# Kernel tuning notes

Measured on AMD Instinct MI355X. Metric: run time of the kernel, lower is better.

Reference implementation:

```python
import jax, jax.numpy as jnp
import numpy as np

IMG, P, CIN, D, K, L, H, FF, B = 512, 32, 3, 256, 8192, 6, 8, 1024, 32
GRID = IMG // P  # 16
DH = D // H
EPS = 1e-5


def _ln(x, w, b):
    m = x.mean(-1, keepdims=True)
    v = ((x - m) ** 2).mean(-1, keepdims=True)
    return (x - m) / jnp.sqrt(v + EPS) * w + b


def _mha(x, wqkv, bqkv, wo, bo):
    # x: (S, Bt, D) -- axis 0 is the attention axis (torch batch_first=False quirk)
    S, Bt, _ = x.shape
    qkv = x @ wqkv.T + bqkv
    q, k, v = jnp.split(qkv, 3, axis=-1)
    q = q.reshape(S, Bt, H, DH)
    k = k.reshape(S, Bt, H, DH)
    v = v.reshape(S, Bt, H, DH)
    scores = jnp.einsum('sbhd,tbhd->bhst', q, k) / jnp.sqrt(jnp.float32(DH))
    attn = jax.nn.softmax(scores, axis=-1)
    o = jnp.einsum('bhst,tbhd->sbhd', attn, v).reshape(S, Bt, D)
    return o @ wo.T + bo


def _conv_t(x, w, b, stride=2, pad=1):
    # w uses torch ConvTranspose2d layout (Cin, Cout, kH, kW)
    kH = w.shape[2]
    wf = jnp.flip(w, (2, 3)).transpose(1, 0, 2, 3)  # -> (Cout, Cin, kH, kW)
    y = jax.lax.conv_general_dilated(
        x, wf, window_strides=(1, 1),
        padding=[(kH - 1 - pad, kH - 1 - pad)] * 2,
        lhs_dilation=(stride, stride),
        dimension_numbers=('NCHW', 'OIHW', 'NCHW'))
    return y + b[None, :, None, None]


def _forward(x, patch_w, patch_b, qkv_w, qkv_b, out_w, out_b, ln1_w, ln1_b,
             ln2_w, ln2_b, ff1_w, ff1_b, ff2_w, ff2_b, lnf_w, lnf_b, codebook,
             dec_w0, dec_b0, dec_w1, dec_b1, dec_w2, dec_b2, dec_w3, dec_b3):
    # patch embedding: conv stride=patch -> (B, D, G, G) -> (B, N, D)
    h = jax.lax.conv_general_dilated(
        x, patch_w, (P, P), 'VALID',
        dimension_numbers=('NCHW', 'OIHW', 'NCHW')) + patch_b[None, :, None, None]
    h = h.reshape(h.shape[0], D, -1).transpose(0, 2, 1)  # (B, N, D)
    # torch TransformerEncoderLayer default batch_first=False: attention runs
    # over axis 0 (image batch); faithfully replicated here. Post-norm, eval
    # mode (dropout=identity), exact gelu.
    for i in range(L):
        a = _mha(h, qkv_w[i], qkv_b[i], out_w[i], out_b[i])
        h = _ln(h + a, ln1_w[i], ln1_b[i])
        f = jax.nn.gelu(h @ ff1_w[i].T + ff1_b[i], approximate=False) @ ff2_w[i].T + ff2_b[i]
        h = _ln(h + f, ln2_w[i], ln2_b[i])
    h = _ln(h, lnf_w, lnf_b)
    # vector quantization: squared-distance argmin over codebook
    flat = h.reshape(-1, D)  # (B*N, D)
    d = ((flat ** 2).sum(-1, keepdims=True)
         - 2.0 * flat @ codebook.T
         + (codebook ** 2).sum(-1))  # (B*N, K)
    idx = jnp.argmin(d, axis=1)
    q = codebook[idx].reshape(h.shape)
    e_loss = jnp.mean((jax.lax.stop_gradient(q) - h) ** 2)
    q_loss = jnp.mean((q - jax.lax.stop_gradient(h)) ** 2)
    vq_loss = q_loss + 0.25 * e_loss
    q = h + jax.lax.stop_gradient(q - h)  # straight-through
    q = q.transpose(0, 2, 1).reshape(x.shape[0], D, GRID, GRID)
    y = jax.nn.relu(_conv_t(q, dec_w0, dec_b0))
    y = jax.nn.relu(_conv_t(y, dec_w1, dec_b1))
    y = jax.nn.relu(_conv_t(y, dec_w2, dec_b2))
    x_hat = jax.nn.sigmoid(_conv_t(y, dec_w3, dec_b3))
    return x_hat, vq_loss


def setup_inputs() -> dict:
    key = jax.random.key(0)
    ks = iter(jax.random.split(key, 64))
    nrm = lambda shape, s=0.02: jax.random.normal(next(ks), shape, jnp.float32) * s
    f32 = jnp.float32
    return {
        'x': jax.random.normal(next(ks), (B, CIN, IMG, IMG), f32),
        'patch_w': nrm((D, CIN, P, P)),
        'patch_b': jnp.zeros((D,), f32),
        'qkv_w': nrm((L, 3 * D, D)),
        'qkv_b': jnp.zeros((L, 3 * D), f32),
        'out_w': nrm((L, D, D)),
        'out_b': jnp.zeros((L, D), f32),
        'ln1_w': jnp.ones((L, D), f32),
        'ln1_b': jnp.zeros((L, D), f32),
        'ln2_w': jnp.ones((L, D), f32),
        'ln2_b': jnp.zeros((L, D), f32),
        'ff1_w': nrm((L, FF, D)),
        'ff1_b': jnp.zeros((L, FF), f32),
        'ff2_w': nrm((L, D, FF)),
        'ff2_b': jnp.zeros((L, D), f32),
        'lnf_w': jnp.ones((D,), f32),
        'lnf_b': jnp.zeros((D,), f32),
        'codebook': jax.random.uniform(next(ks), (K, D), f32, -1.0 / K, 1.0 / K),
        'dec_w0': nrm((D, 256, 4, 4)),
        'dec_b0': jnp.zeros((256,), f32),
        'dec_w1': nrm((256, 128, 4, 4)),
        'dec_b1': jnp.zeros((128,), f32),
        'dec_w2': nrm((128, 64, 4, 4)),
        'dec_b2': jnp.zeros((64,), f32),
        'dec_w3': nrm((64, CIN, 4, 4)),
        'dec_b3': jnp.zeros((CIN,), f32),
    }


def reference(x, patch_w, patch_b, qkv_w, qkv_b, out_w, out_b, ln1_w, ln1_b,
              ln2_w, ln2_b, ff1_w, ff1_b, ff2_w, ff2_b, lnf_w, lnf_b, codebook,
              dec_w0, dec_b0, dec_w1, dec_b1, dec_w2, dec_b2, dec_w3, dec_b3):
    return _forward(x, patch_w, patch_b, qkv_w, qkv_b, out_w, out_b, ln1_w,
                    ln1_b, ln2_w, ln2_b, ff1_w, ff1_b, ff2_w, ff2_b, lnf_w,
                    lnf_b, codebook, dec_w0, dec_b0, dec_w1, dec_b1, dec_w2,
                    dec_b2, dec_w3, dec_b3)
```

## Files before the change

kernel.cpp:

```cpp
#include <hip/hip_runtime.h>
#include <hip/hip_bf16.h>
#include <math.h>

typedef __hip_bfloat16 bf16;
typedef unsigned int u32;
typedef unsigned long long u64;
using short8 = __attribute__((ext_vector_type(8))) short;
using f32x4  = __attribute__((ext_vector_type(4))) float;

__device__ __forceinline__ float b2f(bf16 v){ return __bfloat162float(v); }
__device__ __forceinline__ bf16  f2b(float v){ return __float2bfloat16(v); }
__device__ __forceinline__ float plo(u32 u){ return __uint_as_float(u << 16); }
__device__ __forceinline__ float phi(u32 u){ return __uint_as_float(u & 0xffff0000u); }

__device__ __forceinline__ void gld16(const void* g, void* l)
{
  __builtin_amdgcn_global_load_lds(
      (const __attribute__((address_space(1))) u32*)g,
      (__attribute__((address_space(3))) u32*)l, 16, 0, 0);
}

__global__ void k_detect(const u32* probe, int* flag)
{
  if (threadIdx.x == 0 && blockIdx.x == 0)
    *flag = (*probe == 0x3F800000u) ? 0 : 1;
}

struct PPack { const void* s[25]; u32 off[26]; };
__global__ __launch_bounds__(256) void k_convall(PPack pp, bf16* P, const int* flag)
{
  const u32 i = blockIdx.x * 256 + threadIdx.x;
  if (i >= pp.off[25]) return;
  int lo = 0, hi = 25;
  while (hi - lo > 1) { const int mid = (lo + hi) >> 1; if (i >= pp.off[mid]) lo = mid; else hi = mid; }
  const u32 j = i - pp.off[lo];
  P[i] = *flag ? ((const bf16*)pp.s[lo])[j] : f2b(((const float*)pp.s[lo])[j]);
}

__global__ __launch_bounds__(256) void k_zborder(bf16* buf, int Hp, int C, int nimg)
{
  const int per = 4 * Hp - 4;
  const int c8 = C >> 3;
  const int total = nimg * per * c8;
  const int i = blockIdx.x * 256 + threadIdx.x;
  if (i >= total) return;
  const int ch8 = i % c8;
  const int pb = i / c8;
  const int img = pb / per;
  const int b = pb - img * per;
  int y, x;
  if (b < Hp) { y = 0; x = b; }
  else if (b < 2 * Hp) { y = Hp - 1; x = b - Hp; }
  else {
    const int r = b - 2 * Hp;
    const int side = r / (Hp - 2);
    y = 1 + r - side * (Hp - 2);
    x = side ? (Hp - 1) : 0;
  }
  uint4 z = {0, 0, 0, 0};
  *reinterpret_cast<uint4*>(buf + (((size_t)img * Hp + y) * Hp + x) * C + ch8 * 8) = z;
}

__global__ __launch_bounds__(128) void k_im2col(const void* x, bf16* A, const int* flag)
{
  const int m = blockIdx.y;
  const int k8 = blockIdx.x * 128 + threadIdx.x;
  const int k = k8 * 8;
  const int b = m >> 8, n = m & 255;
  const int gy = n >> 4, gx = n & 15;
  const int c = k >> 10, r = (k >> 5) & 31, pp = k & 31;
  const size_t src = (((size_t)(b * 3 + c) * 512) + gy * 32 + r) * 512 + gx * 32 + pp;
  bf16 ov[8];
  if (*flag) {
    const bf16* xp = (const bf16*)x + src;
    #pragma unroll
    for (int i = 0; i < 8; ++i) ov[i] = xp[i];
  } else {
    const float4 v0 = *reinterpret_cast<const float4*>((const float*)x + src);
    const float4 v1 = *reinterpret_cast<const float4*>((const float*)x + src + 4);
    ov[0]=f2b(v0.x); ov[1]=f2b(v0.y); ov[2]=f2b(v0.z); ov[3]=f2b(v0.w);
    ov[4]=f2b(v1.x); ov[5]=f2b(v1.y); ov[6]=f2b(v1.z); ov[7]=f2b(v1.w);
  }
  *reinterpret_cast<uint4*>(A + (size_t)m * 3072 + k) = *reinterpret_cast<const uint4*>(ov);
}

template<int EPI, int FM, int BN, bool DB>
__global__ __launch_bounds__(256, 2) void gemm_t(
    const bf16* __restrict__ A, const bf16* __restrict__ Bw,
    const bf16* __restrict__ bias, const bf16* res, bf16* C,
    const float* __restrict__ cnorm, u64* __restrict__ ku,
    int M, int N, int K, int Kc)
{
  constexpr int BM = FM * 32;
  constexpr int FN = BN / 32;
  __shared__ alignas(16) bf16 As[DB ? 2 : 1][BM * 64];
  __shared__ alignas(16) bf16 Bs[DB ? 2 : 1][BN * 64];
  const int tid = threadIdx.x;
  const int bn = blockIdx.x * BN, bm = blockIdx.y * BM;
  const int z = blockIdx.z;
  const int kb = z * Kc;
  const int l = tid & 63, w = tid >> 6;
  const int wm = w >> 1, wn = w & 1;
  const int lg = l >> 4, lr = l & 15;
  const int sr8 = l >> 3;
  const int sch = (l & 7) ^ sr8;
  f32x4 acc[FM][FN];
  #pragma unroll
  for (int fm = 0; fm < FM; ++fm)
    #pragma unroll
    for (int fn = 0; fn < FN; ++fn) acc[fm][fn] = (f32x4){0.f, 0.f, 0.f, 0.f};

  auto stage = [&](int bb, int k0) {
    char* ab = (char*)As[bb];
    char* bp = (char*)Bs[bb];
    #pragma unroll
    for (int it = 0; it < FM; ++it) {
      const int r = w * 8 + it * 32 + sr8;
      gld16(A + (size_t)(bm + r) * K + k0 + sch * 8, ab + w * 1024 + it * 4096);
    }
    #pragma unroll
    for (int it = 0; it < BN / 32; ++it) {
      const int r = w * 8 + it * 32 + sr8;
      gld16(Bw + (size_t)(bn + r) * K + k0 + sch * 8, bp + w * 1024 + it * 4096);
    }
  };
  auto compute = [&](int bb) {
    const char* ab = (const char*)As[bb];
    const char* bp = (const char*)Bs[bb];
    #pragma unroll
    for (int ks = 0; ks < 2; ++ks) {
      short8 af[FM], bfr[FN];
      #pragma unroll
      for (int fm = 0; fm < FM; ++fm) {
        const int r = wm * (FM * 16) + fm * 16 + lr;
        af[fm] = *reinterpret_cast<const short8*>(ab + r * 128 + (((lg + ks * 4) ^ (r & 7)) * 16));
      }
      #pragma unroll
      for (int fn = 0; fn < FN; ++fn) {
        const int r = wn * (BN / 2) + fn * 16 + lr;
        bfr[fn] = *reinterpret_cast<const short8*>(bp + r * 128 + (((lg + ks * 4) ^ (r & 7)) * 16));
      }
      #pragma unroll
      for (int fm = 0; fm < FM; ++fm)
        #pragma unroll
        for (int fn = 0; fn < FN; ++fn)
          acc[fm][fn] = __builtin_amdgcn_mfma_f32_16x16x32_bf16(af[fm], bfr[fn], acc[fm][fn], 0, 0, 0);
    }
  };

  const int nt = Kc >> 6;
  if (DB) {
    stage(0, kb);
    __syncthreads();
    for (int t = 0; t < nt; ++t) {
      const int cur = t & 1;
      if (t + 1 < nt) stage(cur ^ 1, kb + ((t + 1) << 6));
      compute(cur);
      __syncthreads();
    }
  } else {
    for (int t = 0; t < nt; ++t) {
      if (t) __syncthreads();
      stage(0, kb + (t << 6));
      __syncthreads();
      compute(0);
    }
  }

  if (EPI == 3) {
    __shared__ u64 skey[BM][2];
    float cn[FN];
    #pragma unroll
    for (int fn = 0; fn < FN; ++fn) cn[fn] = cnorm[bn + wn * (BN / 2) + fn * 16 + lr];
    #pragma unroll
    for (int fm = 0; fm < FM; ++fm) {
      #pragma unroll
      for (int r = 0; r < 4; ++r) {
        u64 best = ~0ull;
        #pragma unroll
        for (int fn = 0; fn < FN; ++fn) {
          const int col = bn + wn * (BN / 2) + fn * 16 + lr;
          const float d = cn[fn] - 2.0f * acc[fm][fn][r];
          u32 u = __float_as_uint(d);
          u = (u & 0x80000000u) ? ~u : (u | 0x80000000u);
          const u64 key = ((u64)u << 32) | (u32)col;
          best = key < best ? key : best;
        }
        #pragma unroll
        for (int mk = 1; mk < 16; mk <<= 1) {
          const u64 o = __shfl_xor(best, mk, 64);
          best = o < best ? o : best;
        }
        if (lr == 0) skey[wm * (FM * 16) + fm * 16 + lg * 4 + r][wn] = best;
      }
    }
    __syncthreads();
    if (tid < BM) {
      const u64 a = skey[tid][0], b = skey[tid][1];
      ku[(size_t)blockIdx.x * M + bm + tid] = a < b ? a : b;
    }
  } else if (EPI == 4) {
    #pragma unroll
    for (int fm = 0; fm < FM; ++fm) {
      const int m0 = bm + wm * (FM * 16) + fm * 16 + lg * 4;
      #pragma unroll
      for (int fn = 0; fn < FN; ++fn) {
        const int n = bn + wn * (BN / 2) + fn * 16 + lr;
        #pragma unroll
        for (int r = 0; r < 4; ++r)
          C[((size_t)z * M + m0 + r) * N + n] = f2b(acc[fm][fn][r]);
      }
    }
  } else {
    #pragma unroll
    for (int fm = 0; fm < FM; ++fm) {
      const int m0 = bm + wm * (FM * 16) + fm * 16 + lg * 4;
      #pragma unroll
      for (int fn = 0; fn < FN; ++fn) {
        const int n = bn + wn * (BN / 2) + fn * 16 + lr;
        const float bs = b2f(bias[n]);
        #pragma unroll
        for (int r = 0; r < 4; ++r) {
          float v = acc[fm][fn][r] + bs;
          if (EPI == 1) v = 0.5f * v * (1.0f + erff(v * 0.70710678118654752f));
          if (EPI == 2) v += b2f(res[(size_t)(m0 + r) * N + n]);
          C[(size_t)(m0 + r) * N + n] = f2b(v);
        }
      }
    }
  }
}

__global__ __launch_bounds__(256, 1) void k_fat1(
    bf16* __restrict__ hbuf,
    const bf16* __restrict__ Wqkv, const bf16* __restrict__ Bqkv,
    const bf16* __restrict__ Wo, const bf16* __restrict__ Bo,
    const bf16* __restrict__ lw, const bf16* __restrict__ lb)
{
  __shared__ alignas(16) bf16 hs[32 * 256];
  __shared__ alignas(16) bf16 ao[32 * 256];
  __shared__ alignas(16) bf16 astage[128 * 64];
  __shared__ bf16 att[3 * 9216];
  __shared__ float ps[32][33];
  __shared__ float rs[32];
  __shared__ float psum[32][4], psq[32][4];
  __shared__ float mstat[32], istat[32];

  const int bt = blockIdx.x;
  const int tid = threadIdx.x;
  const int l = tid & 63, w = tid >> 6;
  const int lg = l >> 4, lr = l & 15;
  const int sr8 = l >> 3;
  const int sch = (l & 7) ^ sr8;
  char* hsb = (char*)hs;
  char* aob = (char*)ao;
  char* asb = (char*)astage;

  #pragma unroll
  for (int call = 0; call < 4; ++call) {
    const int id = call * 256 + tid;
    const int s = id >> 5, within = id & 31;
    const int grp = within >> 3, c = within & 7;
    gld16(hbuf + (size_t)(s * 256 + bt) * 256 + grp * 64 + ((c ^ (s & 7)) * 8),
          hsb + call * 4096 + w * 1024);
  }

  for (int at = 0; at < 6; ++at) {
    f32x4 acc[2][2];
    #pragma unroll
    for (int fm = 0; fm < 2; ++fm)
      #pragma unroll
      for (int fn = 0; fn < 2; ++fn) acc[fm][fn] = (f32x4){0.f, 0.f, 0.f, 0.f};
    for (int kst = 0; kst < 4; ++kst) {
      __syncthreads();
      #pragma unroll
      for (int it = 0; it < 4; ++it) {
        const int r = w * 8 + it * 32 + sr8;
        gld16(Wqkv + (size_t)(at * 128 + r) * 256 + kst * 64 + sch * 8,
              asb + w * 1024 + it * 4096);
      }
      __syncthreads();
      #pragma unroll
      for (int ks = 0; ks < 2; ++ks) {
        short8 af[2], bfr[2];
        #pragma unroll
        for (int fm = 0; fm < 2; ++fm) {
          const int r = w * 32 + fm * 16 + lr;
          af[fm] = *reinterpret_cast<const short8*>(asb + r * 128 + (((lg + ks * 4) ^ (r & 7)) * 16));
        }
        #pragma unroll
        for (int fn = 0; fn < 2; ++fn) {
          const int sr = fn * 16 + lr;
          bfr[fn] = *reinterpret_cast<const short8*>(hsb + sr * 512 + kst * 128 + (((lg + ks * 4) ^ (sr & 7)) * 16));
        }
        #pragma unroll
        for (int fm = 0; fm < 2; ++fm)
          #pragma unroll
          for (int fn = 0; fn < 2; ++fn)
            acc[fm][fn] = __builtin_amdgcn_mfma_f32_16x16x32_bf16(af[fm], bfr[fn], acc[fm][fn], 0, 0, 0);
      }
    }
    #pragma unroll
    for (int fm = 0; fm < 2; ++fm) {
      #pragma unroll
      for (int fn = 0; fn < 2; ++fn) {
        const int s = fn * 16 + lr;
        #pragma unroll
        for (int r = 0; r < 4; ++r) {
          const int n = at * 128 + w * 32 + fm * 16 + lg * 4 + r;
          const int p = n >> 8, rem = n & 255;
          att[p * 9216 + (rem >> 5) * 1152 + s * 36 + (rem & 31)] =
              f2b(acc[fm][fn][r] + b2f(Bqkv[n]));
        }
      }
    }
  }
  __syncthreads();

  const int s_a = tid >> 3, j_a = tid & 7;
  for (int hd = 0; hd < 8; ++hd) {
    const bf16* qrow = att + hd * 1152 + s_a * 36;
    float sc[4];
    #pragma unroll
    for (int e = 0; e < 4; ++e) {
      const int t = j_a + 8 * e;
      const bf16* krow = att + 9216 + hd * 1152 + t * 36;
      float v = 0.f;
      #pragma unroll
      for (int dd = 0; dd < 32; ++dd) v += b2f(qrow[dd]) * b2f(krow[dd]);
      sc[e] = v * 0.17677669529663687f;
    }
    float mx = fmaxf(fmaxf(sc[0], sc[1]), fmaxf(sc[2], sc[3]));
    #pragma unroll
    for (int mk = 1; mk < 8; mk <<= 1) mx = fmaxf(mx, __shfl_xor(mx, mk, 64));
    float sm = 0.f; float ex[4];
    #pragma unroll
    for (int e = 0; e < 4; ++e) { ex[e] = expf(sc[e] - mx); sm += ex[e]; }
    #pragma unroll
    for (int mk = 1; mk < 8; mk <<= 1) sm += __shfl_xor(sm, mk, 64);
    #pragma unroll
    for (int e = 0; e < 4; ++e) ps[s_a][j_a + 8 * e] = ex[e];
    if (j_a == 0) rs[s_a] = 1.0f / sm;
    __syncthreads();
    const float rinv = rs[s_a];
    float av[4];
    #pragma unroll
    for (int e = 0; e < 4; ++e) {
      const int dd = j_a * 4 + e;
      float a = 0.f;
      #pragma unroll
      for (int t = 0; t < 32; ++t)
        a += ps[s_a][t] * b2f(att[2 * 9216 + hd * 1152 + t * 36 + dd]);
      av[e] = a * rinv;
    }
    alignas(8) bf16 ov[4];
    #pragma unroll
    for (int e = 0; e < 4; ++e) ov[e] = f2b(av[e]);
    const int clog = (hd & 1) * 4 + (j_a >> 1);
    *reinterpret_cast<ushort4*>(aob + s_a * 512 + (hd >> 1) * 128 +
        ((clog ^ (s_a & 7)) * 16) + (j_a & 1) * 8) =
        *reinterpret_cast<const ushort4*>(ov);
    __syncthreads();
  }

  float vals[2][2][2][4];
  for (int at = 0; at < 2; ++at) {
    f32x4 acc[2][2];
    #pragma unroll
    for (int fm = 0; fm < 2; ++fm)
      #pragma unroll
      for (int fn = 0; fn < 2; ++fn) acc[fm][fn] = (f32x4){0.f, 0.f, 0.f, 0.f};
    for (int kst = 0; kst < 4; ++kst) {
      __syncthreads();
      #pragma unroll
      for (int it = 0; it < 4; ++it) {
        const int r = w * 8 + it * 32 + sr8;
        gld16(Wo + (size_t)(at * 128 + r) * 256 + kst * 64 + sch * 8,
              asb + w * 1024 + it * 4096);
      }
      __syncthreads();
      #pragma unroll
      for (int ks = 0; ks < 2; ++ks) {
        short8 af[2], bfr[2];
        #pragma unroll
        for (int fm = 0; fm < 2; ++fm) {
          const int r = w * 32 + fm * 16 + lr;
          af[fm] = *reinterpret_cast<const short8*>(asb + r * 128 + (((lg + ks * 4) ^ (r & 7)) * 16));
        }
        #pragma unroll
        for (int fn = 0; fn < 2; ++fn) {
          const int sr = fn * 16 + lr;
          bfr[fn] = *reinterpret_cast<const short8*>(aob + sr * 512 + kst * 128 + (((lg + ks * 4) ^ (sr & 7)) * 16));
        }
        #pragma unroll
        for (int fm = 0; fm < 2; ++fm)
          #pragma unroll
          for (int fn = 0; fn < 2; ++fn)
            acc[fm][fn] = __builtin_amdgcn_mfma_f32_16x16x32_bf16(af[fm], bfr[fn], acc[fm][fn], 0, 0, 0);
      }
    }
    #pragma unroll
    for (int fm = 0; fm < 2; ++fm)
      #pragma unroll
      for (int fn = 0; fn < 2; ++fn)
        #pragma unroll
        for (int r = 0; r < 4; ++r) vals[at][fm][fn][r] = acc[fm][fn][r];
  }

  float s1[2] = {0.f, 0.f}, s2[2] = {0.f, 0.f};
  #pragma unroll
  for (int at = 0; at < 2; ++at) {
    #pragma unroll
    for (int fm = 0; fm < 2; ++fm) {
      const int n4 = at * 128 + w * 32 + fm * 16 + lg * 4;
      #pragma unroll
      for (int fn = 0; fn < 2; ++fn) {
        const int s = fn * 16 + lr;
        const ushort4 hr = *reinterpret_cast<const ushort4*>(
            hsb + s * 512 + (n4 >> 6) * 128 + ((((n4 >> 3) & 7) ^ (s & 7)) * 16) + (n4 & 7) * 2);
        const bf16* hb = reinterpret_cast<const bf16*>(&hr);
        #pragma unroll
        for (int r = 0; r < 4; ++r) {
          const float v = vals[at][fm][fn][r] + b2f(Bo[n4 + r]) + b2f(hb[r]);
          vals[at][fm][fn][r] = v;
          s1[fn] += v;
          s2[fn] += v * v;
        }
      }
    }
  }
  #pragma unroll
  for (int fn = 0; fn < 2; ++fn) {
    float a = s1[fn], b = s2[fn];
    a += __shfl_xor(a, 16, 64); a += __shfl_xor(a, 32, 64);
    b += __shfl_xor(b, 16, 64); b += __shfl_xor(b, 32, 64);
    if (lg == 0) { psum[fn * 16 + lr][w] = a; psq[fn * 16 + lr][w] = b; }
  }
  __syncthreads();
  if (tid < 32) {
    float sa = 0.f, sb = 0.f;
    #pragma unroll
    for (int k = 0; k < 4; ++k) { sa += psum[tid][k]; sb += psq[tid][k]; }
    const float m = sa * (1.0f / 256.0f);
    mstat[tid] = m;
    istat[tid] = 1.0f / sqrtf(sb * (1.0f / 256.0f) - m * m + 1e-5f);
  }
  __syncthreads();
  #pragma unroll
  for (int at = 0; at < 2; ++at) {
    #pragma unroll
    for (int fm = 0; fm < 2; ++fm) {
      const int n4 = at * 128 + w * 32 + fm * 16 + lg * 4;
      #pragma unroll
      for (int fn = 0; fn < 2; ++fn) {
        const int s = fn * 16 + lr;
        const float m = mstat[s], inv = istat[s];
        alignas(8) bf16 ov[4];
        #pragma unroll
        for (int r = 0; r < 4; ++r)
          ov[r] = f2b((vals[at][fm][fn][r] - m) * inv * b2f(lw[n4 + r]) + b2f(lb[n4 + r]));
        *reinterpret_cast<ushort4*>(hbuf + (size_t)(s * 256 + bt) * 256 + n4) =
            *reinterpret_cast<const ushort4*>(ov);
      }
    }
  }
}

template<bool DOLN>
__global__ __launch_bounds__(256) void k_lnred(
    const bf16* __restrict__ Pf, const bf16* __restrict__ bias,
    const bf16* res, const bf16* __restrict__ lw, const bf16* __restrict__ lb,
    bf16* h, int kc)
{
  __shared__ float red[256];
  __shared__ float stat[2];
  const int row = blockIdx.x, d = threadIdx.x;
  float s = 0.f;
  for (int z = 0; z < kc; ++z) s += b2f(Pf[((size_t)z * 8192 + row) * 256 + d]);
  s += b2f(bias[d]);
  if (res) s += b2f(res[(size_t)row * 256 + d]);
  if (!DOLN) { h[(size_t)row * 256 + d] = f2b(s); return; }
  red[d] = s;
  __syncthreads();
  for (int off = 128; off > 0; off >>= 1) {
    if (d < off) red[d] += red[d + off];
    __syncthreads();
  }
  if (d == 0) stat[0] = red[0] * (1.0f / 256.0f);
  __syncthreads();
  const float m = stat[0];
  red[d] = (s - m) * (s - m);
  __syncthreads();
  for (int off = 128; off > 0; off >>= 1) {
    if (d < off) red[d] += red[d + off];
    __syncthreads();
  }
  if (d == 0) stat[1] = 1.0f / sqrtf(red[0] * (1.0f / 256.0f) + 1e-5f);
  __syncthreads();
  h[(size_t)row * 256 + d] = f2b((s - m) * stat[1] * b2f(lw[d]) + b2f(lb[d]));
}

__global__ __launch_bounds__(256) void k_vqmerge(
    const u64* __restrict__ ku, int* __restrict__ idx, int M, int NB)
{
  const int r = blockIdx.x * 256 + threadIdx.x;
  if (r >= M) return;
  u64 best = ku[r];
  for (int nb = 1; nb < NB; ++nb) {
    const u64 k = ku[(size_t)nb * M + r];
    best = k < best ? k : best;
  }
  idx[r] = (int)(best & 0xFFFFFFFFull);
}

__global__ __launch_bounds__(256) void k_cnorm(const bf16* __restrict__ cb, float* __restrict__ cn)
{
  const int j = blockIdx.x * 256 + threadIdx.x;
  const u32* p = (const u32*)(cb + (size_t)j * 256);
  float s = 0.f;
  for (int k = 0; k < 128; ++k) {
    const u32 v = p[k];
    const float a = plo(v), b = phi(v);
    s += a * a + b * b;
  }
  cn[j] = s;
}

__global__ __launch_bounds__(256) void k_ln(
    bf16* h, const bf16* w, const bf16* b)
{
  __shared__ float red[256];
  __shared__ float stat[2];
  const int row = blockIdx.x, d = threadIdx.x;
  const size_t base = (size_t)row * 256;
  const float x = b2f(h[base + d]);
  red[d] = x;
  __syncthreads();
  for (int off = 128; off > 0; off >>= 1) {
    if (d < off) red[d] += red[d + off];
    __syncthreads();
  }
  if (d == 0) stat[0] = red[0] * (1.0f / 256.0f);
  __syncthreads();
  const float m = stat[0];
  red[d] = (x - m) * (x - m);
  __syncthreads();
  for (int off = 128; off > 0; off >>= 1) {
    if (d < off) red[d] += red[d + off];
    __syncthreads();
  }
  if (d == 0) stat[1] = 1.0f / sqrtf(red[0] * (1.0f / 256.0f) + 1e-5f);
  __syncthreads();
  h[base + d] = f2b((x - m) * stat[1] * b2f(w[d]) + b2f(b[d]));
}

__global__ __launch_bounds__(256) void k_gather(
    const bf16* h, const bf16* cb, const int* idx, bf16* a0, float* lsum)
{
  __shared__ float red[256];
  const int row = blockIdx.x, d = threadIdx.x;
  const int code = idx[row] & 8191;
  const float q = b2f(cb[(size_t)code * 256 + d]);
  const float x = b2f(h[(size_t)row * 256 + d]);
  red[d] = (q - x) * (q - x);
  __syncthreads();
  for (int off = 128; off > 0; off >>= 1) {
    if (d < off) red[d] += red[d + off];
    __syncthreads();
  }
  if (d == 0) lsum[row] = red[0];
  const int b = row >> 8, n = row & 255;
  const int y = n >> 4, xc = n & 15;
  a0[(((size_t)b * 18 + y + 1) * 18 + (xc + 1)) * 256 + d] = f2b(q);
}

__global__ __launch_bounds__(256) void k_loss(const float* lsum, float* out)
{
  __shared__ float red[256];
  const int tid = threadIdx.x;
  float v = 0.f;
  for (int i = 0; i < 32; ++i) v += lsum[tid + 256 * i];
  red[tid] = v;
  __syncthreads();
  for (int off = 128; off > 0; off >>= 1) {
    if (tid < off) red[tid] += red[tid + off];
    __syncthreads();
  }
  if (tid == 0)
    out[0] = red[0] * (1.25f / 2097152.0f);
}

__global__ __launch_bounds__(256) void k_wtrans(
    const bf16* __restrict__ w, bf16* __restrict__ wt,
    int Cin, int lCin, int CoutR, int CoutP)
{
  const int K = Cin << 2;
  const int total = 4 * CoutP * K;
  const int i = blockIdx.x * 256 + threadIdx.x;
  if (i >= total) return;
  const int p = i / (CoutP * K);
  const int rem = i - p * (CoutP * K);
  const int co = rem / K;
  const int k = rem - co * K;
  const int tap = k >> lCin, ci = k - (tap << lCin);
  const int py = p >> 1, px = p & 1, ty = tap >> 1, tx = tap & 1;
  bf16 v = f2b(0.f);
  if (co < CoutR)
    v = w[(((size_t)ci * CoutR + co) * 4 + py + 2 * ty) * 4 + px + 2 * tx];
  wt[i] = v;
}

__global__ __launch_bounds__(256, 2) void convt64(
    const bf16* __restrict__ in, const bf16* __restrict__ Wt,
    const bf16* __restrict__ bias, bf16* __restrict__ outp,
    int H, int lH, int Cin, int lCin, int Cout)
{
  __shared__ alignas(16) bf16 As[2][128 * 64];
  __shared__ alignas(16) bf16 Bs[2][64 * 64];
  const int tid = threadIdx.x;
  const int pz = blockIdx.z;
  const int py = pz >> 1, px = pz & 1;
  const int K = Cin << 2;
  const int bn = blockIdx.x * 64, bm = blockIdx.y * 128;
  const bf16* Bw = Wt + (size_t)pz * Cout * K;
  const int l = tid & 63, w = tid >> 6;
  const int wm = w >> 1, wn = w & 1;
  const int lg = l >> 4, lr = l & 15;
  const int sr8 = l >> 3;
  const int sch = (l & 7) ^ sr8;
  const int Hp = H + 2;
  f32x4 acc[4][2];
  #pragma unroll
  for (int fm = 0; fm < 4; ++fm)
    #pragma unroll
    for (int fn = 0; fn < 2; ++fn) acc[fm][fn] = (f32x4){0.f, 0.f, 0.f, 0.f};

  size_t pixbase[4];
  #pragma unroll
  for (int it = 0; it < 4; ++it) {
    const int m = bm + w * 8 + it * 32 + sr8;
    const int b = m >> (2 * lH);
    const int rem = m & ((1 << (2 * lH)) - 1);
    const int jj = rem >> lH, ii = rem & (H - 1);
    pixbase[it] = ((size_t)(b * Hp + jj) * Hp + ii);
  }

  auto stage = [&](int bb, int k0) {
    char* ab = (char*)As[bb];
    char* bp = (char*)Bs[bb];
    const int tap = k0 >> lCin;
    const int ty = tap >> 1, tx = tap & 1;
    const int sy = (1 - py) + (1 - ty);
    const int sx = (1 - px) + (1 - tx);
    const int ci0 = (k0 - (tap << lCin)) + sch * 8;
    #pragma unroll
    for (int it = 0; it < 4; ++it)
      gld16(in + (pixbase[it] + (size_t)sy * Hp + sx) * Cin + ci0,
            ab + w * 1024 + it * 4096);
    #pragma unroll
    for (int it = 0; it < 2; ++it) {
      const int r = w * 8 + it * 32 + sr8;
      gld16(Bw + (size_t)(bn + r) * K + k0 + sch * 8, bp + w * 1024 + it * 4096);
    }
  };

  const int nt = K >> 6;
  stage(0, 0);
  __syncthreads();
  for (int t = 0; t < nt; ++t) {
    const int cur = t & 1;
    if (t + 1 < nt) stage(cur ^ 1, (t + 1) << 6);
    const char* ab = (const char*)As[cur];
    const char* bb = (const char*)Bs[cur];
    #pragma unroll
    for (int ks = 0; ks < 2; ++ks) {
      short8 af[4], bfr[2];
      #pragma unroll
      for (int fm = 0; fm < 4; ++fm) {
        const int r = wm * 64 + fm * 16 + lr;
        af[fm] = *reinterpret_cast<const short8*>(ab + r * 128 + (((lg + ks * 4) ^ (r & 7)) * 16));
      }
      #pragma unroll
      for (int fn = 0; fn < 2; ++fn) {
        const int r = wn * 32 + fn * 16 + lr;
        bfr[fn] = *reinterpret_cast<const short8*>(bb + r * 128 + (((lg + ks * 4) ^ (r & 7)) * 16));
      }
      #pragma unroll
      for (int fm = 0; fm < 4; ++fm)
        #pragma unroll
        for (int fn = 0; fn < 2; ++fn)
          acc[fm][fn] = __builtin_amdgcn_mfma_f32_16x16x32_bf16(af[fm], bfr[fn], acc[fm][fn], 0, 0, 0);
    }
    __syncthreads();
  }

  const int Ho = 2 * H, Hop = Ho + 2;
  #pragma unroll
  for (int fm = 0; fm < 4; ++fm) {
    const int m0 = bm + wm * 64 + fm * 16 + lg * 4;
    #pragma unroll
    for (int fn = 0; fn < 2; ++fn) {
      const int n = bn + wn * 32 + fn * 16 + lr;
      #pragma unroll
      for (int r = 0; r < 4; ++r) {
        const int m = m0 + r;
        const int b = m >> (2 * lH);
        const int rem = m & ((1 << (2 * lH)) - 1);
        const int jj = rem >> lH, ii = rem & (H - 1);
        const int oy = 2 * jj + (1 - py), ox = 2 * ii + (1 - px);
        const float v = fmaxf(acc[fm][fn][r] + b2f(bias[n]), 0.f);
        outp[((size_t)(b * Hop + oy + 1) * Hop + ox + 1) * Cout + n] = f2b(v);
      }
    }
  }
}

__global__ __launch_bounds__(256) void k_dec3(
    const bf16* __restrict__ a3, const bf16* __restrict__ wt3,
    const bf16* __restrict__ bias, float* __restrict__ xhat, int chunkBase)
{
  __shared__ float wl[3][264];
  const int tid = threadIdx.x;
  const int pz = blockIdx.y;
  const int py = pz >> 1, px = pz & 1;
  for (int i = tid; i < 768; i += 256) {
    const int co = i >> 8, k = i & 255;
    wl[co][k] = b2f(wt3[(pz * 3 + co) * 256 + k]);
  }
  __syncthreads();
  const int b = blockIdx.z;
  const int p = blockIdx.x * 64 + (tid >> 2);
  const int jj = p >> 7, ii = p & 127;
  const int ch4 = tid & 3;
  float a0 = 0.f, a1 = 0.f, a2 = 0.f;
  #pragma unroll
  for (int ty = 0; ty < 2; ++ty) {
    #pragma unroll
    for (int tx = 0; tx < 2; ++tx) {
      const int sy = (1 - py) + (1 - ty), sx = (1 - px) + (1 - tx);
      const int tap = ty * 2 + tx;
      const u32* ip = (const u32*)(a3 + ((size_t)(b * 130 + jj + sy) * 130 + ii + sx) * 64) + ch4 * 8;
      const float* w0 = &wl[0][tap * 64 + ch4 * 16];
      const float* w1 = &wl[1][tap * 64 + ch4 * 16];
      const float* w2 = &wl[2][tap * 64 + ch4 * 16];
      #pragma unroll
      for (int kk = 0; kk < 8; ++kk) {
        const u32 v = ip[kk];
        const float e0 = plo(v), e1 = phi(v);
        a0 += e0 * w0[2 * kk] + e1 * w0[2 * kk + 1];
        a1 += e0 * w1[2 * kk] + e1 * w1[2 * kk + 1];
        a2 += e0 * w2[2 * kk] + e1 * w2[2 * kk + 1];
      }
    }
  }
  a0 += __shfl_xor(a0, 1, 64); a0 += __shfl_xor(a0, 2, 64);
  a1 += __shfl_xor(a1, 1, 64); a1 += __shfl_xor(a1, 2, 64);
  a2 += __shfl_xor(a2, 1, 64); a2 += __shfl_xor(a2, 2, 64);
  if (ch4 < 3) {
    const float av = ch4 == 0 ? a0 : (ch4 == 1 ? a1 : a2);
    const int oy = 2 * jj + (1 - py), ox = 2 * ii + (1 - px);
    const float t = av + b2f(bias[ch4]);
    xhat[(((size_t)(chunkBase + b) * 3 + ch4) * 256 + oy) * 256 + ox] =
        1.0f / (1.0f + expf(-t));
  }
}

extern "C" void kernel_launch(void* const* d_in, const int* in_sizes, int n_in,
                              void* d_out, int out_size, void* d_ws, size_t ws_size,
                              hipStream_t stream)
{
  float* xhat = (float*)d_out;
  float* lossout = xhat + (out_size - 1);

  const size_t NEED = 130195456;
  if (ws_size < NEED) return;

  char* ws = (char*)d_ws;
  int*   flag  = (int*)  (ws + 0);
  float* lsum  = (float*)(ws + 1024);
  int*   idx   = (int*)  (ws + 65536);
  u64*   ku    = (u64*)  (ws + 131072);
  bf16*  P     = (bf16*) (ws + 8519680);
  bf16*  WT    = (bf16*) (ws + 27262976);
  float* cnorm = (float*)(ws + 30900224);
  bf16*  hbuf  = (bf16*) (ws + 31457280);
  bf16*  A_im  = (bf16*) (ws + 35651584);
  bf16*  ffb   = (bf16*) (ws + 52428800);
  bf16*  Pfb   = (bf16*) (ws + 85983232);
  bf16*  a0    = (bf16*) (ws + 35651584);
  bf16*  a1    = (bf16*) (ws + 40960000);
  bf16*  a2    = (bf16*) (ws + 59899904);
  bf16*  a3    = (bf16*) (ws + 95584256);

  k_detect<<<1, 64, 0, stream>>>((const u32*)d_in[7], flag);

  size_t poff[26]; poff[1] = 0;
  for (int i = 2; i <= 25; ++i) poff[i] = poff[i - 1] + (size_t)in_sizes[i - 1];
  const size_t ptotal = poff[25] + (size_t)in_sizes[25];
  PPack pp;
  for (int i = 0; i < 25; ++i) { pp.s[i] = d_in[i + 1]; pp.off[i] = (u32)poff[i + 1]; }
  pp.off[25] = (u32)ptotal;
  k_convall<<<(int)((ptotal + 255) / 256), 256, 0, stream>>>(pp, P, flag);

  const bf16 *patch_w = P + poff[1],  *patch_b = P + poff[2];
  const bf16 *qkv_w   = P + poff[3],  *qkv_b   = P + poff[4];
  const bf16 *out_w   = P + poff[5],  *out_b   = P + poff[6];
  const bf16 *ln1_w   = P + poff[7],  *ln1_b   = P + poff[8];
  const bf16 *ln2_w   = P + poff[9],  *ln2_b   = P + poff[10];
  const bf16 *ff1_w   = P + poff[11], *ff1_b   = P + poff[12];
  const bf16 *ff2_w   = P + poff[13], *ff2_b   = P + poff[14];
  const bf16 *lnf_w   = P + poff[15], *lnf_b   = P + poff[16];
  const bf16 *codebook= P + poff[17];
  const bf16 *dec_w0  = P + poff[18], *dec_b0  = P + poff[19];
  const bf16 *dec_w1  = P + poff[20], *dec_b1  = P + poff[21];
  const bf16 *dec_w2  = P + poff[22], *dec_b2  = P + poff[23];
  const bf16 *dec_w3  = P + poff[24], *dec_b3  = P + poff[25];

  bf16* wt0 = WT;
  bf16* wt1 = wt0 + 1048576;
  bf16* wt2 = wt1 + 524288;
  bf16* wt3 = wt2 + 131072;
  k_wtrans<<<(1048576 + 255) / 256, 256, 0, stream>>>(dec_w0, wt0, 256, 8, 256, 256);
  k_wtrans<<<(524288 + 255) / 256, 256, 0, stream>>>(dec_w1, wt1, 256, 8, 128, 128);
  k_wtrans<<<(131072 + 255) / 256, 256, 0, stream>>>(dec_w2, wt2, 128, 7, 64, 64);
  k_wtrans<<<(3072 + 255) / 256, 256, 0, stream>>>(dec_w3, wt3, 64, 6, 3, 3);
  k_cnorm<<<32, 256, 0, stream>>>(codebook, cnorm);

  k_im2col<<<dim3(3, 8192), 128, 0, stream>>>(d_in[0], A_im, flag);
  gemm_t<4, 2, 128, true><<<dim3(2, 128, 4), 256, 0, stream>>>(
      A_im, patch_w, nullptr, nullptr, Pfb, nullptr, nullptr, 8192, 256, 3072, 768);
  k_lnred<false><<<8192, 256, 0, stream>>>(
      Pfb, patch_b, nullptr, nullptr, nullptr, hbuf, 4);

  for (int l = 0; l < 6; ++l) {
    k_fat1<<<256, 256, 0, stream>>>(
        hbuf, qkv_w + (size_t)l * 768 * 256, qkv_b + l * 768,
        out_w + (size_t)l * 256 * 256, out_b + l * 256,
        ln1_w + l * 256, ln1_b + l * 256);
    gemm_t<1, 2, 256, false><<<dim3(4, 128, 1), 256, 0, stream>>>(
        hbuf, ff1_w + (size_t)l * 1024 * 256, ff1_b + l * 1024, nullptr, ffb,
        nullptr, nullptr, 8192, 1024, 256, 256);
    gemm_t<4, 2, 128, false><<<dim3(2, 128, 4), 256, 0, stream>>>(
        ffb, ff2_w + (size_t)l * 256 * 1024, nullptr, nullptr, Pfb,
        nullptr, nullptr, 8192, 256, 1024, 256);
    k_lnred<true><<<8192, 256, 0, stream>>>(
        Pfb, ff2_b + l * 256, hbuf, ln2_w + l * 256, ln2_b + l * 256, hbuf, 4);
  }
  k_ln<<<8192, 256, 0, stream>>>(hbuf, lnf_w, lnf_b);

  gemm_t<3, 2, 256, false><<<dim3(32, 128, 1), 256, 0, stream>>>(
      hbuf, codebook, nullptr, nullptr, nullptr, cnorm, ku, 8192, 8192, 256, 256);
  k_vqmerge<<<32, 256, 0, stream>>>(ku, idx, 8192, 32);

  k_zborder<<<(32 * 68 * 32 + 255) / 256, 256, 0, stream>>>(a0, 18, 256, 32);
  k_gather<<<8192, 256, 0, stream>>>(hbuf, codebook, idx, a0, lsum);
  k_loss<<<1, 256, 0, stream>>>(lsum, lossout);
  k_zborder<<<(32 * 132 * 32 + 255) / 256, 256, 0, stream>>>(a1, 34, 256, 32);
  k_zborder<<<(32 * 260 * 16 + 255) / 256, 256, 0, stream>>>(a2, 66, 128, 32);
  k_zborder<<<(16 * 516 * 8 + 255) / 256, 256, 0, stream>>>(a3, 130, 64, 16);

  convt64<<<dim3(4, 64, 4), 256, 0, stream>>>(a0, wt0, dec_b0, a1, 16, 4, 256, 8, 256);
  convt64<<<dim3(2, 256, 4), 256, 0, stream>>>(a1, wt1, dec_b1, a2, 32, 5, 256, 8, 128);
  for (int c = 0; c < 2; ++c) {
    const bf16* a2c = a2 + (size_t)c * 16 * 66 * 66 * 128;
    convt64<<<dim3(1, 512, 4), 256, 0, stream>>>(a2c, wt2, dec_b2, a3, 64, 6, 128, 7, 64);
    k_dec3<<<dim3(256, 4, 16), 256, 0, stream>>>(a3, wt3, dec_b3, xhat, c * 16);
  }
}
```

Measured before the change: 973.9 us.

## Fuse FFN up-projection, GELU, down-projection and LayerNorm into one kernel

Replaces the FF1 GEMM, the split-K FF2 GEMM and the reduce+LayerNorm kernel with a single kernel per 32-token block. The GELU intermediate stays in LDS and is never written to global memory, which removes the ffb and split-K partial traffic and two launches per layer. In exchange there are only 256 blocks, one per CU under launch_bounds(256,1), each using about 100KB of LDS. Each block streams all weights through a double-buffered 128x64 stage, so weight traffic grows and the hardware may be underoccupied.

```diff
diff --git a/kernel.cpp b/kernel.cpp
--- a/kernel.cpp
+++ b/kernel.cpp
@@ -466,6 +466,210 @@
   }
 }
 
+__global__ __launch_bounds__(256, 1) void k_fft(
+    bf16* __restrict__ hbuf,
+    const bf16* __restrict__ W1, const bf16* __restrict__ B1,
+    const bf16* __restrict__ W2, const bf16* __restrict__ B2,
+    const bf16* __restrict__ lw, const bf16* __restrict__ lb)
+{
+  __shared__ alignas(16) bf16 hs[32 * 256];
+  __shared__ alignas(16) bf16 G[32 * 1024];
+  __shared__ alignas(16) bf16 astage[2][128 * 64];
+  __shared__ float psum[32][4], psq[32][4];
+  __shared__ float mstat[32], istat[32];
+
+  const int blk = blockIdx.x;
+  const int tid = threadIdx.x;
+  const int l = tid & 63, w = tid >> 6;
+  const int lg = l >> 4, lr = l & 15;
+  const int sr8 = l >> 3;
+  const int sch = (l & 7) ^ sr8;
+  char* hsb = (char*)hs;
+  char* Gb = (char*)G;
+
+  #pragma unroll
+  for (int call = 0; call < 4; ++call) {
+    const int id = call * 256 + tid;
+    const int s = id >> 5, within = id & 31;
+    const int grp = within >> 3, c = within & 7;
+    gld16(hbuf + (size_t)(blk * 32 + s) * 256 + grp * 64 + ((c ^ (s & 7)) * 8),
+          hsb + call * 4096 + w * 1024);
+  }
+
+  auto stageW = [&](int bb, const bf16* W, int row0, int kst, int ldk) {
+    char* ab = (char*)astage[bb];
+    #pragma unroll
+    for (int it = 0; it < 4; ++it) {
+      const int r = w * 8 + it * 32 + sr8;
+      gld16(W + (size_t)(row0 + r) * ldk + kst * 64 + sch * 8,
+            ab + w * 1024 + it * 4096);
+    }
+  };
+
+  {
+    f32x4 acc[2][2];
+    stageW(0, W1, 0, 0, 256);
+    __syncthreads();
+    for (int g = 0; g < 32; ++g) {
+      const int at = g >> 2, kst = g & 3;
+      const int cur = g & 1;
+      if (g + 1 < 32) stageW(cur ^ 1, W1, ((g + 1) >> 2) * 128, (g + 1) & 3, 256);
+      if (kst == 0) {
+        #pragma unroll
+        for (int fm = 0; fm < 2; ++fm)
+          #pragma unroll
+          for (int fn = 0; fn < 2; ++fn) acc[fm][fn] = (f32x4){0.f, 0.f, 0.f, 0.f};
+      }
+      const char* ab = (const char*)astage[cur];
+      #pragma unroll
+      for (int ks = 0; ks < 2; ++ks) {
+        short8 af[2], bfr[2];
+        #pragma unroll
+        for (int fm = 0; fm < 2; ++fm) {
+          const int r = w * 32 + fm * 16 + lr;
+          af[fm] = *reinterpret_cast<const short8*>(ab + r * 128 + (((lg + ks * 4) ^ (r & 7)) * 16));
+        }
+        #pragma unroll
+        for (int fn = 0; fn < 2; ++fn) {
+          const int sr = fn * 16 + lr;
+          bfr[fn] = *reinterpret_cast<const short8*>(hsb + sr * 512 + kst * 128 + (((lg + ks * 4) ^ (sr & 7)) * 16));
+        }
+        #pragma unroll
+        for (int fm = 0; fm < 2; ++fm)
+          #pragma unroll
+          for (int fn = 0; fn < 2; ++fn)
+            acc[fm][fn] = __builtin_amdgcn_mfma_f32_16x16x32_bf16(af[fm], bfr[fn], acc[fm][fn], 0, 0, 0);
+      }
+      if (kst == 3) {
+        #pragma unroll
+        for (int fm = 0; fm < 2; ++fm) {
+          const int n4 = at * 128 + w * 32 + fm * 16 + lg * 4;
+          #pragma unroll
+          for (int fn = 0; fn < 2; ++fn) {
+            const int s = fn * 16 + lr;
+            alignas(8) bf16 ov[4];
+            #pragma unroll
+            for (int r = 0; r < 4; ++r) {
+              float v = acc[fm][fn][r] + b2f(B1[n4 + r]);
+              v = 0.5f * v * (1.0f + erff(v * 0.70710678118654752f));
+              ov[r] = f2b(v);
+            }
+            *reinterpret_cast<ushort4*>(Gb + s * 2048 + (n4 >> 6) * 128 +
+                ((((n4 >> 3) & 7) ^ (s & 7)) * 16) + (n4 & 7) * 2) =
+                *reinterpret_cast<const ushort4*>(ov);
+          }
+        }
+      }
+      __syncthreads();
+    }
+  }
+
+  float vals[2][2][2][4];
+  {
+    f32x4 acc[2][2];
+    stageW(0, W2, 0, 0, 1024);
+    __syncthreads();
+    for (int g = 0; g < 32; ++g) {
+      const int at = g >> 4, kst = g & 15;
+      const int cur = g & 1;
+      if (g + 1 < 32) stageW(cur ^ 1, W2, ((g + 1) >> 4) * 128, (g + 1) & 15, 1024);
+      if (kst == 0) {
+        #pragma unroll
+        for (int fm = 0; fm < 2; ++fm)
+          #pragma unroll
+          for (int fn = 0; fn < 2; ++fn) acc[fm][fn] = (f32x4){0.f, 0.f, 0.f, 0.f};
+      }
+      const char* ab = (const char*)astage[cur];
+      #pragma unroll
+      for (int ks = 0; ks < 2; ++ks) {
+        short8 af[2], bfr[2];
+        #pragma unroll
+        for (int fm = 0; fm < 2; ++fm) {
+          const int r = w * 32 + fm * 16 + lr;
+          af[fm] = *reinterpret_cast<const short8*>(ab + r * 128 + (((lg + ks * 4) ^ (r & 7)) * 16));
+        }
+        #pragma unroll
+        for (int fn = 0; fn < 2; ++fn) {
+          const int sr = fn * 16 + lr;
+          bfr[fn] = *reinterpret_cast<const short8*>(Gb + sr * 2048 + kst * 128 + (((lg + ks * 4) ^ (sr & 7)) * 16));
+        }
+        #pragma unroll
+        for (int fm = 0; fm < 2; ++fm)
+          #pragma unroll
+          for (int fn = 0; fn < 2; ++fn)
+            acc[fm][fn] = __builtin_amdgcn_mfma_f32_16x16x32_bf16(af[fm], bfr[fn], acc[fm][fn], 0, 0, 0);
+      }
+      if (kst == 15) {
+        #pragma unroll
+        for (int fm = 0; fm < 2; ++fm)
+          #pragma unroll
+          for (int fn = 0; fn < 2; ++fn)
+            #pragma unroll
+            for (int r = 0; r < 4; ++r) vals[at][fm][fn][r] = acc[fm][fn][r];
+      }
+      __syncthreads();
+    }
+  }
+
+  float s1[2] = {0.f, 0.f}, s2[2] = {0.f, 0.f};
+  #pragma unroll
+  for (int at = 0; at < 2; ++at) {
+    #pragma unroll
+    for (int fm = 0; fm < 2; ++fm) {
+      const int n4 = at * 128 + w * 32 + fm * 16 + lg * 4;
+      #pragma unroll
+      for (int fn = 0; fn < 2; ++fn) {
+        const int s = fn * 16 + lr;
+        const ushort4 hr = *reinterpret_cast<const ushort4*>(
+            hsb + s * 512 + (n4 >> 6) * 128 + ((((n4 >> 3) & 7) ^ (s & 7)) * 16) + (n4 & 7) * 2);
+        const bf16* hb = reinterpret_cast<const bf16*>(&hr);
+        #pragma unroll
+        for (int r = 0; r < 4; ++r) {
+          const float v = vals[at][fm][fn][r] + b2f(B2[n4 + r]) + b2f(hb[r]);
+          vals[at][fm][fn][r] = v;
+          s1[fn] += v;
+          s2[fn] += v * v;
+        }
+      }
+    }
+  }
+  #pragma unroll
+  for (int fn = 0; fn < 2; ++fn) {
+    float a = s1[fn], b = s2[fn];
+    a += __shfl_xor(a, 16, 64); a += __shfl_xor(a, 32, 64);
+    b += __shfl_xor(b, 16, 64); b += __shfl_xor(b, 32, 64);
+    if (lg == 0) { psum[fn * 16 + lr][w] = a; psq[fn * 16 + lr][w] = b; }
+  }
+  __syncthreads();
+  if (tid < 32) {
+    float sa = 0.f, sb = 0.f;
+    #pragma unroll
+    for (int k = 0; k < 4; ++k) { sa += psum[tid][k]; sb += psq[tid][k]; }
+    const float m = sa * (1.0f / 256.0f);
+    mstat[tid] = m;
+    istat[tid] = 1.0f / sqrtf(sb * (1.0f / 256.0f) - m * m + 1e-5f);
+  }
+  __syncthreads();
+  #pragma unroll
+  for (int at = 0; at < 2; ++at) {
+    #pragma unroll
+    for (int fm = 0; fm < 2; ++fm) {
+      const int n4 = at * 128 + w * 32 + fm * 16 + lg * 4;
+      #pragma unroll
+      for (int fn = 0; fn < 2; ++fn) {
+        const int s = fn * 16 + lr;
+        const float m = mstat[s], inv = istat[s];
+        alignas(8) bf16 ov[4];
+        #pragma unroll
+        for (int r = 0; r < 4; ++r)
+          ov[r] = f2b((vals[at][fm][fn][r] - m) * inv * b2f(lw[n4 + r]) + b2f(lb[n4 + r]));
+        *reinterpret_cast<ushort4*>(hbuf + (size_t)(blk * 32 + s) * 256 + n4) =
+            *reinterpret_cast<const ushort4*>(ov);
+      }
+    }
+  }
+}
+
 template<bool DOLN>
 __global__ __launch_bounds__(256) void k_lnred(
     const bf16* __restrict__ Pf, const bf16* __restrict__ bias,
@@ -785,7 +989,6 @@
   float* cnorm = (float*)(ws + 30900224);
   bf16*  hbuf  = (bf16*) (ws + 31457280);
   bf16*  A_im  = (bf16*) (ws + 35651584);
-  bf16*  ffb   = (bf16*) (ws + 52428800);
   bf16*  Pfb   = (bf16*) (ws + 85983232);
   bf16*  a0    = (bf16*) (ws + 35651584);
   bf16*  a1    = (bf16*) (ws + 40960000);
@@ -837,14 +1040,10 @@
         hbuf, qkv_w + (size_t)l * 768 * 256, qkv_b + l * 768,
         out_w + (size_t)l * 256 * 256, out_b + l * 256,
         ln1_w + l * 256, ln1_b + l * 256);
-    gemm_t<1, 2, 256, false><<<dim3(4, 128, 1), 256, 0, stream>>>(
-        hbuf, ff1_w + (size_t)l * 1024 * 256, ff1_b + l * 1024, nullptr, ffb,
-        nullptr, nullptr, 8192, 1024, 256, 256);
-    gemm_t<4, 2, 128, false><<<dim3(2, 128, 4), 256, 0, stream>>>(
-        ffb, ff2_w + (size_t)l * 256 * 1024, nullptr, nullptr, Pfb,
-        nullptr, nullptr, 8192, 256, 1024, 256);
-    k_lnred<true><<<8192, 256, 0, stream>>>(
-        Pfb, ff2_b + l * 256, hbuf, ln2_w + l * 256, ln2_b + l * 256, hbuf, 4);
+    k_fft<<<256, 256, 0, stream>>>(
+        hbuf, ff1_w + (size_t)l * 1024 * 256, ff1_b + l * 1024,
+        ff2_w + (size_t)l * 256 * 1024, ff2_b + l * 256,
+        ln2_w + l * 256, ln2_b + l * 256);
   }
   k_ln<<<8192, 256, 0, stream>>>(hbuf, lnf_w, lnf_b);
 
```

Result: slower. 1.041 ms (+6.9%).
